# Kernel optimization log

Hardware: AMD Instinct MI355X
Metric: run time of the kernel (lower is better)

Reference implementation:

```python
import jax, jax.numpy as jnp
import numpy as np

B, T, C, H = 4, 2048, 1024, 16
HD = C // H


def setup_inputs() -> dict:
    key = jax.random.key(0)
    k1, k2, k3, k4 = jax.random.split(key, 4)
    x = jax.random.normal(k1, (B, T, C), dtype=jnp.float32)
    pad_mask = jnp.ones((B, T), dtype=jnp.int32)
    # Linear weights stored as (in, out); torch Linear uses W.T so math is identical.
    w_attn = jax.random.normal(k2, (C, 3 * C), dtype=jnp.float32) * (1.0 / np.sqrt(C))
    w_proj = jax.random.normal(k3, (C, C), dtype=jnp.float32) * (1.0 / np.sqrt(C))
    b_proj = jax.random.normal(k4, (C,), dtype=jnp.float32) * 0.01
    return {"x": x, "pad_mask": pad_mask, "w_attn": w_attn, "w_proj": w_proj, "b_proj": b_proj}


def reference(x, pad_mask, w_attn, w_proj, b_proj):
    Bx, Tx, Cx = x.shape
    hd = Cx // H
    qkv = x @ w_attn                                  # (B,T,3C)
    q, k, v = jnp.split(qkv, 3, axis=2)
    # (B,T,C) -> (B,H,T,hd)
    q = q.reshape(Bx, Tx, H, hd).transpose(0, 2, 1, 3)
    k = k.reshape(Bx, Tx, H, hd).transpose(0, 2, 1, 3)
    v = v.reshape(Bx, Tx, H, hd).transpose(0, 2, 1, 3)
    att = jnp.einsum('bhqd,bhkd->bhqk', q, k) * (1.0 / np.sqrt(hd))
    causal = jnp.tril(jnp.ones((Tx, Tx), dtype=bool))[None, None]       # (1,1,T,T)
    keep = causal & (pad_mask[:, None, None, :] != 0)                   # (B,1,T,T) broadcast
    att = jnp.where(keep, att, -jnp.inf)
    att = jax.nn.softmax(att, axis=-1)
    # dropout p=0.0 (eval) -> identity
    y = jnp.einsum('bhqk,bhkd->bhqd', att, v)
    y = y.transpose(0, 2, 1, 3).reshape(Bx, Tx, Cx)
    return y @ w_proj + b_proj
```

## Files before the change

kernel.cpp:

```cpp
#include <hip/hip_runtime.h>
#include <hip/hip_bf16.h>


using short8  = __attribute__((ext_vector_type(8))) short;
using short4_ = __attribute__((ext_vector_type(4))) short;
using uint2_  = __attribute__((ext_vector_type(2))) unsigned int;
using float4_ = __attribute__((ext_vector_type(4))) float;

#define Bb   4
#define Tt   2048
#define Cc   1024
#define Hh   16
#define HDd  64

__device__ __forceinline__ float bf2f(unsigned short u) {
    union { float f; unsigned int i; } x; x.i = ((unsigned int)u) << 16; return x.f;
}
__device__ __forceinline__ unsigned short f2bf(float f) {
    union { float f; unsigned int i; } x; x.f = f;
    unsigned int r = x.i + 0x7fff + ((x.i >> 16) & 1);
    return (unsigned short)(r >> 16);
}
__device__ __forceinline__ unsigned int cvtpk_bf16(float lo, float hi) {
    unsigned int r;
    asm("v_cvt_pk_bf16_f32 %0, %1, %2" : "=v"(r) : "v"(lo), "v"(hi));
    return r;
}
__device__ __forceinline__ float4_ bmfma(short8 a, short8 b, float4_ c) {
    return __builtin_amdgcn_mfma_f32_16x16x32_bf16(a, b, c, 0, 0, 0);
}
__device__ __forceinline__ float ex2(float x) {
    return __builtin_amdgcn_exp2f(x);
}
__device__ __forceinline__ void gl2lds16(const unsigned short* g, unsigned short* l) {
    __builtin_amdgcn_global_load_lds(
        (const __attribute__((address_space(1))) void*)g,
        (__attribute__((address_space(3))) void*)l, 16, 0, 0);
}

__global__ __launch_bounds__(256) void convert_f32_bf16(
    const float* __restrict__ in, unsigned short* __restrict__ out)
{
    size_t idx = ((size_t)blockIdx.x * 256 + threadIdx.x) * 8;
    float4_ f0 = *(const float4_*)&in[idx];
    float4_ f1 = *(const float4_*)&in[idx + 4];
    short8 h;
    h[0] = (short)f2bf(f0[0]); h[1] = (short)f2bf(f0[1]);
    h[2] = (short)f2bf(f0[2]); h[3] = (short)f2bf(f0[3]);
    h[4] = (short)f2bf(f1[0]); h[5] = (short)f2bf(f1[1]);
    h[6] = (short)f2bf(f1[2]); h[7] = (short)f2bf(f1[3]);
    *(short8*)&out[idx] = h;
}

__global__ __launch_bounds__(256) void transpose_f32_bf16(
    const float* __restrict__ in, unsigned short* __restrict__ out,
    int R, int Ccols)
{
    __shared__ unsigned short tile[32][33];
    int c0 = blockIdx.x * 32, r0 = blockIdx.y * 32;
    int tx = threadIdx.x & 31, ty = threadIdx.x >> 5;
    for (int o = 0; o < 32; o += 8)
        tile[ty + o][tx] = f2bf(in[(size_t)(r0 + ty + o) * Ccols + c0 + tx]);
    __syncthreads();
    for (int o = 0; o < 32; o += 8)
        out[(size_t)(c0 + ty + o) * R + r0 + tx] = tile[tx][ty + o];
}

#define GBK 64

__device__ __forceinline__ void gemm128_main(
    const unsigned short* __restrict__ A, const unsigned short* __restrict__ Bt,
    int K, int m0, int n0,
    unsigned short* As, unsigned short* Bs, float4_ acc[4][4], bool swapT)
{
    int tid  = threadIdx.x;
    int wave = tid >> 6, lane = tid & 63;
    int wm = (wave >> 1) * 64, wn = (wave & 1) * 64;
    int lr = lane & 15, lg = lane >> 4;
    int srow = tid >> 3;
    int scol = (tid & 7) * 8;

    for (int k0 = 0; k0 < K; k0 += GBK) {
        #pragma unroll
        for (int j = 0; j < 4; j++) {
            int row = j * 32 + srow;
            gl2lds16(&A [(size_t)(m0 + row) * K + k0 + scol], &As[row * GBK + scol]);
            gl2lds16(&Bt[(size_t)(n0 + row) * K + k0 + scol], &Bs[row * GBK + scol]);
        }
        __syncthreads();
        #pragma unroll
        for (int ks = 0; ks < GBK; ks += 32) {
            short8 af[4], bf[4];
            #pragma unroll
            for (int i = 0; i < 4; i++) {
                af[i] = *(const short8*)&As[(wm + i * 16 + lr) * GBK + ks + lg * 8];
                bf[i] = *(const short8*)&Bs[(wn + i * 16 + lr) * GBK + ks + lg * 8];
            }
            if (!swapT) {
                #pragma unroll
                for (int i = 0; i < 4; i++)
                    #pragma unroll
                    for (int j = 0; j < 4; j++)
                        acc[i][j] = bmfma(af[i], bf[j], acc[i][j]);
            } else {
                #pragma unroll
                for (int i = 0; i < 4; i++)
                    #pragma unroll
                    for (int j = 0; j < 4; j++)
                        acc[i][j] = bmfma(bf[i], af[j], acc[i][j]);
            }
        }
        __syncthreads();
    }
}

__device__ __forceinline__ void supertile_remap(int& m0, int& n0)
{
    int bx = blockIdx.x, by = blockIdx.y;
    int mt = ((by & 7) << 3) | (bx & 7);
    int nt = ((by >> 3) << 3) | (bx >> 3);
    m0 = mt * 128; n0 = nt * 128;
}

__global__ __launch_bounds__(256) void gemm_qkv(
    const unsigned short* __restrict__ A,
    const unsigned short* __restrict__ Bt,
    unsigned short* __restrict__ Q,
    unsigned short* __restrict__ Ko,
    unsigned short* __restrict__ V)
{
    __shared__ unsigned short As[128 * GBK];
    __shared__ unsigned short Bs[128 * GBK];
    int m0, n0;
    supertile_remap(m0, n0);
    bool vblk = (n0 >= 2048);
    float4_ acc[4][4] = {};
    gemm128_main(A, Bt, 1024, m0, n0, As, Bs, acc, vblk);

    int lane = threadIdx.x & 63, wave = threadIdx.x >> 6;
    int wm = (wave >> 1) * 64, wn = (wave & 1) * 64;
    int lr = lane & 15, lg = lane >> 4;
    if (!vblk) {
        #pragma unroll
        for (int i = 0; i < 4; i++)
            #pragma unroll
            for (int j = 0; j < 4; j++) {
                int n = n0 + wn + 16 * j + lr;
                int which = n >> 10;
                int c = n & 1023;
                int h = c >> 6, d = c & 63;
                unsigned short* dst = (which == 0) ? Q : Ko;
                float sc2 = (which == 0) ? 0.1803368801f : 1.0f;
                #pragma unroll
                for (int r = 0; r < 4; r++) {
                    int m = m0 + wm + 16 * i + lg * 4 + r;
                    int b = m >> 11, t = m & 2047;
                    dst[(((size_t)(b * Hh + h) * Tt) + t) * HDd + d] = f2bf(acc[i][j][r] * sc2);
                }
            }
    } else {
        #pragma unroll
        for (int i = 0; i < 4; i++)
            #pragma unroll
            for (int j = 0; j < 4; j++) {
                int m = m0 + wm + 16 * j + lr;
                int b = m >> 11, t = m & 2047;
                #pragma unroll
                for (int r = 0; r < 4; r++) {
                    int n = n0 + wn + 16 * i + lg * 4 + r;
                    int c = n - 2048;
                    int h = c >> 6, d = c & 63;
                    V[(((size_t)(b * Hh + h) * HDd) + d) * Tt + t] = f2bf(acc[i][j][r]);
                }
            }
    }
}

__global__ __launch_bounds__(256) void gemm_proj(
    const unsigned short* __restrict__ A,
    const unsigned short* __restrict__ Bt,
    const float* __restrict__ bias,
    float* __restrict__ Out)
{
    __shared__ unsigned short As[128 * GBK];
    __shared__ unsigned short Bs[128 * GBK];
    int m0, n0;
    supertile_remap(m0, n0);
    float4_ acc[4][4] = {};
    gemm128_main(A, Bt, 1024, m0, n0, As, Bs, acc, false);

    int lane = threadIdx.x & 63, wave = threadIdx.x >> 6;
    int wm = (wave >> 1) * 64, wn = (wave & 1) * 64;
    int lr = lane & 15, lg = lane >> 4;
    #pragma unroll
    for (int i = 0; i < 4; i++)
        #pragma unroll
        for (int j = 0; j < 4; j++) {
            int n = n0 + wn + 16 * j + lr;
            float bv = bias[n];
            #pragma unroll
            for (int r = 0; r < 4; r++) {
                int m = m0 + wm + 16 * i + lg * 4 + r;
                Out[(size_t)m * 1024 + n] = acc[i][j][r] + bv;
            }
        }
}

#define DPAD 72

__global__ __launch_bounds__(256) void attn_fwd(
    const unsigned short* __restrict__ Q,
    const unsigned short* __restrict__ Kg,
    const unsigned short* __restrict__ Vg,
    const int* __restrict__ pad,
    unsigned short* __restrict__ Y)
{
    __shared__ unsigned short smem[4 * 64 * DPAD];

    int flat = blockIdx.x;
    int qb = 31 - (flat >> 6);
    int bh = flat & 63;
    int b  = bh >> 4, h = bh & 15;
    const size_t base = (size_t)bh * Tt * HDd;
    int tid  = threadIdx.x;
    int wave = tid >> 6, lane = tid & 63;
    int lr = lane & 15, lg = lane >> 4;
    int q0 = qb * 64 + wave * 16;
    const int* padRow = pad + b * Tt;

    int r8 = tid >> 3;
    int c8 = (tid & 7) * 8;

    short8 qf0 = *(const short8*)&Q[base + (size_t)(q0 + lr) * HDd + lg * 8];
    short8 qf1 = *(const short8*)&Q[base + (size_t)(q0 + lr) * HDd + 32 + lg * 8];

    float m_i = -1e30f, l_i = 0.f;
    float4_ o_acc[4];
    #pragma unroll
    for (int dt = 0; dt < 4; dt++) o_acc[dt] = (float4_){0.f, 0.f, 0.f, 0.f};

    int ebase = (lg & 1) * 4;
    int hnib  = lg >> 1;
    int q2    = (2 * lr) & 7;

    short8 kr0 = *(const short8*)&Kg[base + (size_t)r8 * HDd + c8];
    short8 kr1 = *(const short8*)&Kg[base + (size_t)(r8 + 32) * HDd + c8];
    short8 vr0 = *(const short8*)&Vg[base + (size_t)r8 * Tt + c8];
    short8 vr1 = *(const short8*)&Vg[base + (size_t)(r8 + 32) * Tt + c8];
    int pvld = padRow[lane];

    for (int kt = 0; kt <= qb; kt++) {
        int cur = kt & 1;
        unsigned short* Kt = smem + cur * (2 * 64 * DPAD);
        unsigned short* Vt = Kt + 64 * DPAD;
        *(short8*)&Kt[r8 * DPAD + c8]        = kr0;
        *(short8*)&Kt[(r8 + 32) * DPAD + c8] = kr1;
        *(short8*)&Vt[r8 * DPAD + c8]        = vr0;
        *(short8*)&Vt[(r8 + 32) * DPAD + c8] = vr1;
        unsigned long long pm = __ballot(pvld != 0);
        __syncthreads();

        if (kt < qb) {
            int k1 = kt * 64 + 64;
            kr0 = *(const short8*)&Kg[base + (size_t)(k1 + r8) * HDd + c8];
            kr1 = *(const short8*)&Kg[base + (size_t)(k1 + r8 + 32) * HDd + c8];
            vr0 = *(const short8*)&Vg[base + (size_t)r8 * Tt + k1 + c8];
            vr1 = *(const short8*)&Vg[base + (size_t)(r8 + 32) * Tt + k1 + c8];
            pvld = padRow[k1 + lane];
        }

        float4_ s[4];
        #pragma unroll
        for (int nt = 0; nt < 4; nt++) {
            short8 kf0 = *(const short8*)&Kt[(nt * 16 + lr) * DPAD + lg * 8];
            short8 kf1 = *(const short8*)&Kt[(nt * 16 + lr) * DPAD + 32 + lg * 8];
            float4_ a = (float4_){0.f, 0.f, 0.f, 0.f};
            a = bmfma(kf0, qf0, a);
            a = bmfma(kf1, qf1, a);
            s[nt] = a;
        }
        if (kt == qb) {
            #pragma unroll
            for (int nt = 0; nt < 4; nt++)
                #pragma unroll
                for (int r = 0; r < 4; r++) {
                    int kl = nt * 16 + lg * 4 + r;
                    bool kpv = (pm >> kl) & 1ull;
                    if (!kpv || kl > wave * 16 + lr) s[nt][r] = -1e30f;
                }
        } else if (pm != ~0ull) {
            #pragma unroll
            for (int nt = 0; nt < 4; nt++)
                #pragma unroll
                for (int r = 0; r < 4; r++) {
                    int kl = nt * 16 + lg * 4 + r;
                    bool kpv = (pm >> kl) & 1ull;
                    s[nt][r] = kpv ? s[nt][r] : -1e30f;
                }
        }
        float v = fmaxf(fmaxf(s[0][0], s[0][1]), fmaxf(s[0][2], s[0][3]));
        #pragma unroll
        for (int nt = 1; nt < 4; nt++)
            v = fmaxf(v, fmaxf(fmaxf(s[nt][0], s[nt][1]), fmaxf(s[nt][2], s[nt][3])));
        v = fmaxf(v, __shfl_xor(v, 16, 64));
        v = fmaxf(v, __shfl_xor(v, 32, 64));
        bool need = __any(v > m_i + 8.0f);
        float alpha = 1.0f;
        if (need) {
            float m_new = fmaxf(m_i, v);
            alpha = ex2(m_i - m_new);
            m_i = m_new;
        }
        float rsum = 0.f;
        #pragma unroll
        for (int nt = 0; nt < 4; nt++)
            #pragma unroll
            for (int r = 0; r < 4; r++) {
                float p = ex2(s[nt][r] - m_i);
                s[nt][r] = p;
                rsum += p;
            }
        rsum += __shfl_xor(rsum, 16, 64);
        rsum += __shfl_xor(rsum, 32, 64);
        l_i = l_i * alpha + rsum;

        if (need) {
            #pragma unroll
            for (int r = 0; r < 4; r++) {
                float ar = __shfl(alpha, (lg << 2) + r, 64);
                #pragma unroll
                for (int dt = 0; dt < 4; dt++)
                    o_acc[dt][r] *= ar;
            }
        }

        __syncthreads();

        unsigned short* Pw = &Kt[wave * 16 * DPAD];
        #pragma unroll
        for (int nt = 0; nt < 4; nt++) {
            uint2_ w;
            w[0] = cvtpk_bf16(s[nt][0], s[nt][1]);
            w[1] = cvtpk_bf16(s[nt][2], s[nt][3]);
            int p = (2 * nt + hnib - q2) & 7;
            *(uint2_*)&Pw[lr * DPAD + p * 8 + ebase] = w;
        }
        short8 pf0 = *(const short8*)&Pw[lr * DPAD + (((lg - q2) & 7) << 3)];
        short8 pf1 = *(const short8*)&Pw[lr * DPAD + (((4 + lg - q2) & 7) << 3)];
        #pragma unroll
        for (int dt = 0; dt < 4; dt++) {
            int d = dt * 16 + lr;
            short8 vf0 = *(const short8*)&Vt[d * DPAD + lg * 8];
            short8 vf1 = *(const short8*)&Vt[d * DPAD + 32 + lg * 8];
            o_acc[dt] = bmfma(pf0, vf0, o_acc[dt]);
            o_acc[dt] = bmfma(pf1, vf1, o_acc[dt]);
        }
    }

    #pragma unroll
    for (int r = 0; r < 4; r++) {
        float lr_ = __shfl(l_i, (lg << 2) + r, 64);
        int qrow = q0 + lg * 4 + r;
        #pragma unroll
        for (int dt = 0; dt < 4; dt++)
            Y[((size_t)b * Tt + qrow) * Cc + h * HDd + dt * 16 + lr] =
                f2bf(o_acc[dt][r] / lr_);
    }
}

extern "C" void kernel_launch(void* const* d_in, const int* in_sizes, int n_in,
                              void* d_out, int out_size, void* d_ws, size_t ws_size,
                              hipStream_t stream)
{
    const float* x      = (const float*)d_in[0];
    const int*   pad    = (const int*)d_in[1];
    const float* w_attn = (const float*)d_in[2];
    const float* w_proj = (const float*)d_in[3];
    const float* b_proj = (const float*)d_in[4];
    float*       out    = (float*)d_out;

    unsigned short* Wta = (unsigned short*)d_ws;
    unsigned short* Wtp = Wta + (size_t)3072 * 1024;
    unsigned short* Xb  = Wtp + (size_t)1024 * 1024;
    unsigned short* Yb  = Xb;
    unsigned short* Qb  = Xb + (size_t)8192 * 1024;
    unsigned short* Kb  = Qb + (size_t)Bb * Hh * Tt * HDd;
    unsigned short* Vb  = Kb + (size_t)Bb * Hh * Tt * HDd;

    convert_f32_bf16<<<dim3(4096), 256, 0, stream>>>(x, Xb);
    transpose_f32_bf16<<<dim3(3072 / 32, 1024 / 32), 256, 0, stream>>>(w_attn, Wta, 1024, 3072);
    transpose_f32_bf16<<<dim3(1024 / 32, 1024 / 32), 256, 0, stream>>>(w_proj, Wtp, 1024, 1024);
    gemm_qkv<<<dim3(8192 / 128, 3072 / 128), 256, 0, stream>>>(Xb, Wta, Qb, Kb, Vb);
    attn_fwd<<<dim3(2048), 256, 0, stream>>>(Qb, Kb, Vb, pad, Yb);
    gemm_proj<<<dim3(8192 / 128, 1024 / 128), 256, 0, stream>>>(Yb, Wtp, b_proj, out);
}
```

Measured before the change: 275.9 us.

## Process two 16-row query tiles per wave in attention to reuse K/V tiles

The attention kernel now gives each block 128 query rows instead of 64, so each wave handles two 16-row query tiles (A and B) against every K/V tile staged in shared memory. This halves the number of blocks and the global-to-LDS K/V traffic per query row, and makes more MFMA work available per sync. Causal masking now covers the last two diagonal tiles using a key offset. The cost is roughly double the accumulator and score registers per thread, which may lower occupancy. Parallelism also drops to 1024 blocks, with coarser causal load imbalance.

After: 282.8 us. 2.5% more time.

```diff
diff --git a/kernel.cpp b/kernel.cpp
--- a/kernel.cpp
+++ b/kernel.cpp
@@ -218,30 +218,37 @@
     __shared__ unsigned short smem[4 * 64 * DPAD];
 
     int flat = blockIdx.x;
-    int qb = 31 - (flat >> 6);
+    int qb = 15 - (flat >> 6);
     int bh = flat & 63;
     int b  = bh >> 4, h = bh & 15;
     const size_t base = (size_t)bh * Tt * HDd;
     int tid  = threadIdx.x;
     int wave = tid >> 6, lane = tid & 63;
     int lr = lane & 15, lg = lane >> 4;
-    int q0 = qb * 64 + wave * 16;
+    int qwA = qb * 128 + wave * 32;
     const int* padRow = pad + b * Tt;
 
     int r8 = tid >> 3;
     int c8 = (tid & 7) * 8;
 
-    short8 qf0 = *(const short8*)&Q[base + (size_t)(q0 + lr) * HDd + lg * 8];
-    short8 qf1 = *(const short8*)&Q[base + (size_t)(q0 + lr) * HDd + 32 + lg * 8];
-
-    float m_i = -1e30f, l_i = 0.f;
-    float4_ o_acc[4];
+    short8 qfA0 = *(const short8*)&Q[base + (size_t)(qwA + lr) * HDd + lg * 8];
+    short8 qfA1 = *(const short8*)&Q[base + (size_t)(qwA + lr) * HDd + 32 + lg * 8];
+    short8 qfB0 = *(const short8*)&Q[base + (size_t)(qwA + 16 + lr) * HDd + lg * 8];
+    short8 qfB1 = *(const short8*)&Q[base + (size_t)(qwA + 16 + lr) * HDd + 32 + lg * 8];
+
+    float mA = -1e30f, lA = 0.f, mB = -1e30f, lB = 0.f;
+    float4_ oA[4], oB[4];
     #pragma unroll
-    for (int dt = 0; dt < 4; dt++) o_acc[dt] = (float4_){0.f, 0.f, 0.f, 0.f};
+    for (int dt = 0; dt < 4; dt++) {
+        oA[dt] = (float4_){0.f, 0.f, 0.f, 0.f};
+        oB[dt] = (float4_){0.f, 0.f, 0.f, 0.f};
+    }
 
     int ebase = (lg & 1) * 4;
     int hnib  = lg >> 1;
     int q2    = (2 * lr) & 7;
+
+    int NT = 2 * qb + 2;
 
     short8 kr0 = *(const short8*)&Kg[base + (size_t)r8 * HDd + c8];
     short8 kr1 = *(const short8*)&Kg[base + (size_t)(r8 + 32) * HDd + c8];
@@ -249,7 +256,7 @@
     short8 vr1 = *(const short8*)&Vg[base + (size_t)(r8 + 32) * Tt + c8];
     int pvld = padRow[lane];
 
-    for (int kt = 0; kt <= qb; kt++) {
+    for (int kt = 0; kt < NT; kt++) {
         int cur = kt & 1;
         unsigned short* Kt = smem + cur * (2 * 64 * DPAD);
         unsigned short* Vt = Kt + 64 * DPAD;
@@ -260,7 +267,7 @@
         unsigned long long pm = __ballot(pvld != 0);
         __syncthreads();
 
-        if (kt < qb) {
+        if (kt < NT - 1) {
             int k1 = kt * 64 + 64;
             kr0 = *(const short8*)&Kg[base + (size_t)(k1 + r8) * HDd + c8];
             kr1 = *(const short8*)&Kg[base + (size_t)(k1 + r8 + 32) * HDd + c8];
@@ -269,24 +276,30 @@
             pvld = padRow[k1 + lane];
         }
 
-        float4_ s[4];
+        float4_ sA[4], sB[4];
         #pragma unroll
         for (int nt = 0; nt < 4; nt++) {
             short8 kf0 = *(const short8*)&Kt[(nt * 16 + lr) * DPAD + lg * 8];
             short8 kf1 = *(const short8*)&Kt[(nt * 16 + lr) * DPAD + 32 + lg * 8];
             float4_ a = (float4_){0.f, 0.f, 0.f, 0.f};
-            a = bmfma(kf0, qf0, a);
-            a = bmfma(kf1, qf1, a);
-            s[nt] = a;
-        }
-        if (kt == qb) {
+            a = bmfma(kf0, qfA0, a);
+            a = bmfma(kf1, qfA1, a);
+            sA[nt] = a;
+            float4_ c = (float4_){0.f, 0.f, 0.f, 0.f};
+            c = bmfma(kf0, qfB0, c);
+            c = bmfma(kf1, qfB1, c);
+            sB[nt] = c;
+        }
+        if (kt >= 2 * qb) {
+            int dk = (kt - 2 * qb) * 64;
             #pragma unroll
             for (int nt = 0; nt < 4; nt++)
                 #pragma unroll
                 for (int r = 0; r < 4; r++) {
                     int kl = nt * 16 + lg * 4 + r;
                     bool kpv = (pm >> kl) & 1ull;
-                    if (!kpv || kl > wave * 16 + lr) s[nt][r] = -1e30f;
+                    if (!kpv || dk + kl > wave * 32 + lr)      sA[nt][r] = -1e30f;
+                    if (!kpv || dk + kl > wave * 32 + 16 + lr) sB[nt][r] = -1e30f;
                 }
         } else if (pm != ~0ull) {
             #pragma unroll
@@ -295,43 +308,59 @@
                 for (int r = 0; r < 4; r++) {
                     int kl = nt * 16 + lg * 4 + r;
                     bool kpv = (pm >> kl) & 1ull;
-                    s[nt][r] = kpv ? s[nt][r] : -1e30f;
+                    if (!kpv) { sA[nt][r] = -1e30f; sB[nt][r] = -1e30f; }
                 }
         }
-        float v = fmaxf(fmaxf(s[0][0], s[0][1]), fmaxf(s[0][2], s[0][3]));
-        #pragma unroll
-        for (int nt = 1; nt < 4; nt++)
-            v = fmaxf(v, fmaxf(fmaxf(s[nt][0], s[nt][1]), fmaxf(s[nt][2], s[nt][3])));
-        v = fmaxf(v, __shfl_xor(v, 16, 64));
-        v = fmaxf(v, __shfl_xor(v, 32, 64));
-        bool need = __any(v > m_i + 8.0f);
-        float alpha = 1.0f;
+        float vA = fmaxf(fmaxf(sA[0][0], sA[0][1]), fmaxf(sA[0][2], sA[0][3]));
+        float vB = fmaxf(fmaxf(sB[0][0], sB[0][1]), fmaxf(sB[0][2], sB[0][3]));
+        #pragma unroll
+        for (int nt = 1; nt < 4; nt++) {
+            vA = fmaxf(vA, fmaxf(fmaxf(sA[nt][0], sA[nt][1]), fmaxf(sA[nt][2], sA[nt][3])));
+            vB = fmaxf(vB, fmaxf(fmaxf(sB[nt][0], sB[nt][1]), fmaxf(sB[nt][2], sB[nt][3])));
+        }
+        vA = fmaxf(vA, __shfl_xor(vA, 16, 64));
+        vA = fmaxf(vA, __shfl_xor(vA, 32, 64));
+        vB = fmaxf(vB, __shfl_xor(vB, 16, 64));
+        vB = fmaxf(vB, __shfl_xor(vB, 32, 64));
+        bool need = __any(vA > mA + 8.0f) || __any(vB > mB + 8.0f);
+        float aA = 1.0f, aB = 1.0f;
         if (need) {
-            float m_new = fmaxf(m_i, v);
-            alpha = ex2(m_i - m_new);
-            m_i = m_new;
-        }
-        float rsum = 0.f;
+            float mnA = fmaxf(mA, vA); aA = ex2(mA - mnA); mA = mnA;
+            float mnB = fmaxf(mB, vB); aB = ex2(mB - mnB); mB = mnB;
+        }
+        float rsA = 0.f, rsB = 0.f;
         #pragma unroll
         for (int nt = 0; nt < 4; nt++)
             #pragma unroll
             for (int r = 0; r < 4; r++) {
-                float p = ex2(s[nt][r] - m_i);
-                s[nt][r] = p;
-                rsum += p;
-            }
-        rsum += __shfl_xor(rsum, 16, 64);
-        rsum += __shfl_xor(rsum, 32, 64);
-        l_i = l_i * alpha + rsum;
-
+                float pA = ex2(sA[nt][r] - mA); sA[nt][r] = pA; rsA += pA;
+                float pB = ex2(sB[nt][r] - mB); sB[nt][r] = pB; rsB += pB;
+            }
+        rsA += __shfl_xor(rsA, 16, 64);
+        rsA += __shfl_xor(rsA, 32, 64);
+        rsB += __shfl_xor(rsB, 16, 64);
+        rsB += __shfl_xor(rsB, 32, 64);
+        lA = lA * aA + rsA;
+        lB = lB * aB + rsB;
         if (need) {
             #pragma unroll
             for (int r = 0; r < 4; r++) {
-                float ar = __shfl(alpha, (lg << 2) + r, 64);
-                #pragma unroll
-                for (int dt = 0; dt < 4; dt++)
-                    o_acc[dt][r] *= ar;
-            }
+                float arA = __shfl(aA, (lg << 2) + r, 64);
+                float arB = __shfl(aB, (lg << 2) + r, 64);
+                #pragma unroll
+                for (int dt = 0; dt < 4; dt++) {
+                    oA[dt][r] *= arA;
+                    oB[dt][r] *= arB;
+                }
+            }
+        }
+        uint2_ wPA[4], wPB[4];
+        #pragma unroll
+        for (int nt = 0; nt < 4; nt++) {
+            wPA[nt][0] = cvtpk_bf16(sA[nt][0], sA[nt][1]);
+            wPA[nt][1] = cvtpk_bf16(sA[nt][2], sA[nt][3]);
+            wPB[nt][0] = cvtpk_bf16(sB[nt][0], sB[nt][1]);
+            wPB[nt][1] = cvtpk_bf16(sB[nt][2], sB[nt][3]);
         }
 
         __syncthreads();
@@ -339,32 +368,43 @@
         unsigned short* Pw = &Kt[wave * 16 * DPAD];
         #pragma unroll
         for (int nt = 0; nt < 4; nt++) {
-            uint2_ w;
-            w[0] = cvtpk_bf16(s[nt][0], s[nt][1]);
-            w[1] = cvtpk_bf16(s[nt][2], s[nt][3]);
             int p = (2 * nt + hnib - q2) & 7;
-            *(uint2_*)&Pw[lr * DPAD + p * 8 + ebase] = w;
-        }
-        short8 pf0 = *(const short8*)&Pw[lr * DPAD + (((lg - q2) & 7) << 3)];
-        short8 pf1 = *(const short8*)&Pw[lr * DPAD + (((4 + lg - q2) & 7) << 3)];
+            *(uint2_*)&Pw[lr * DPAD + p * 8 + ebase] = wPA[nt];
+        }
+        short8 pfA0 = *(const short8*)&Pw[lr * DPAD + (((lg - q2) & 7) << 3)];
+        short8 pfA1 = *(const short8*)&Pw[lr * DPAD + (((4 + lg - q2) & 7) << 3)];
+        #pragma unroll
+        for (int nt = 0; nt < 4; nt++) {
+            int p = (2 * nt + hnib - q2) & 7;
+            *(uint2_*)&Pw[lr * DPAD + p * 8 + ebase] = wPB[nt];
+        }
+        short8 pfB0 = *(const short8*)&Pw[lr * DPAD + (((lg - q2) & 7) << 3)];
+        short8 pfB1 = *(const short8*)&Pw[lr * DPAD + (((4 + lg - q2) & 7) << 3)];
         #pragma unroll
         for (int dt = 0; dt < 4; dt++) {
             int d = dt * 16 + lr;
             short8 vf0 = *(const short8*)&Vt[d * DPAD + lg * 8];
             short8 vf1 = *(const short8*)&Vt[d * DPAD + 32 + lg * 8];
-            o_acc[dt] = bmfma(pf0, vf0, o_acc[dt]);
-            o_acc[dt] = bmfma(pf1, vf1, o_acc[dt]);
+            oA[dt] = bmfma(pfA0, vf0, oA[dt]);
+            oA[dt] = bmfma(pfA1, vf1, oA[dt]);
+            oB[dt] = bmfma(pfB0, vf0, oB[dt]);
+            oB[dt] = bmfma(pfB1, vf1, oB[dt]);
         }
     }
 
     #pragma unroll
     for (int r = 0; r < 4; r++) {
-        float lr_ = __shfl(l_i, (lg << 2) + r, 64);
-        int qrow = q0 + lg * 4 + r;
-        #pragma unroll
-        for (int dt = 0; dt < 4; dt++)
-            Y[((size_t)b * Tt + qrow) * Cc + h * HDd + dt * 16 + lr] =
-                f2bf(o_acc[dt][r] / lr_);
+        float lAr = __shfl(lA, (lg << 2) + r, 64);
+        float lBr = __shfl(lB, (lg << 2) + r, 64);
+        int qrA = qwA + lg * 4 + r;
+        int qrB = qwA + 16 + lg * 4 + r;
+        #pragma unroll
+        for (int dt = 0; dt < 4; dt++) {
+            Y[((size_t)b * Tt + qrA) * Cc + h * HDd + dt * 16 + lr] =
+                f2bf(oA[dt][r] / lAr);
+            Y[((size_t)b * Tt + qrB) * Cc + h * HDd + dt * 16 + lr] =
+                f2bf(oB[dt][r] / lBr);
+        }
     }
 }
 
@@ -391,6 +431,6 @@
     transpose_f32_bf16<<<dim3(3072 / 32, 1024 / 32), 256, 0, stream>>>(w_attn, Wta, 1024, 3072);
     transpose_f32_bf16<<<dim3(1024 / 32, 1024 / 32), 256, 0, stream>>>(w_proj, Wtp, 1024, 1024);
     gemm_qkv<<<dim3(8192 / 128, 3072 / 128), 256, 0, stream>>>(Xb, Wta, Qb, Kb, Vb);
-    attn_fwd<<<dim3(2048), 256, 0, stream>>>(Qb, Kb, Vb, pad, Yb);
+    attn_fwd<<<dim3(1024), 256, 0, stream>>>(Qb, Kb, Vb, pad, Yb);
     gemm_proj<<<dim3(8192 / 128, 1024 / 128), 256, 0, stream>>>(Yb, Wtp, b_proj, out);
 }
```

## Load K/V MFMA fragments directly from global memory, drop LDS staging

Applied to the files above, without the earlier changes.

The attention kernel stops staging K and V tiles in shared memory with register prefetch and block-wide barriers. Each wave now reads its K and V MFMA fragments straight from global memory, and shared memory holds only the per-wave P tile. This removes the two __syncthreads per iteration and the LDS write/read traffic, and the smaller LDS footprint may allow more blocks per CU. In exchange, each of the four waves loads the same K/V data separately, which quadruples global/L2 traffic, and the software prefetch overlap is lost.

Result: slower. 452.5 us (+64.0%).

```diff
diff --git a/kernel.cpp b/kernel.cpp
--- a/kernel.cpp
+++ b/kernel.cpp
@@ -215,7 +215,7 @@
     const int* __restrict__ pad,
     unsigned short* __restrict__ Y)
 {
-    __shared__ unsigned short smem[4 * 64 * DPAD];
+    __shared__ unsigned short Psm[4 * 16 * DPAD];
 
     int flat = blockIdx.x;
     int qb = 31 - (flat >> 6);
@@ -227,9 +227,7 @@
     int lr = lane & 15, lg = lane >> 4;
     int q0 = qb * 64 + wave * 16;
     const int* padRow = pad + b * Tt;
-
-    int r8 = tid >> 3;
-    int c8 = (tid & 7) * 8;
+    unsigned short* Pw = &Psm[wave * 16 * DPAD];
 
     short8 qf0 = *(const short8*)&Q[base + (size_t)(q0 + lr) * HDd + lg * 8];
     short8 qf1 = *(const short8*)&Q[base + (size_t)(q0 + lr) * HDd + 32 + lg * 8];
@@ -243,42 +241,23 @@
     int hnib  = lg >> 1;
     int q2    = (2 * lr) & 7;
 
-    short8 kr0 = *(const short8*)&Kg[base + (size_t)r8 * HDd + c8];
-    short8 kr1 = *(const short8*)&Kg[base + (size_t)(r8 + 32) * HDd + c8];
-    short8 vr0 = *(const short8*)&Vg[base + (size_t)r8 * Tt + c8];
-    short8 vr1 = *(const short8*)&Vg[base + (size_t)(r8 + 32) * Tt + c8];
-    int pvld = padRow[lane];
-
     for (int kt = 0; kt <= qb; kt++) {
-        int cur = kt & 1;
-        unsigned short* Kt = smem + cur * (2 * 64 * DPAD);
-        unsigned short* Vt = Kt + 64 * DPAD;
-        *(short8*)&Kt[r8 * DPAD + c8]        = kr0;
-        *(short8*)&Kt[(r8 + 32) * DPAD + c8] = kr1;
-        *(short8*)&Vt[r8 * DPAD + c8]        = vr0;
-        *(short8*)&Vt[(r8 + 32) * DPAD + c8] = vr1;
-        unsigned long long pm = __ballot(pvld != 0);
-        __syncthreads();
-
-        if (kt < qb) {
-            int k1 = kt * 64 + 64;
-            kr0 = *(const short8*)&Kg[base + (size_t)(k1 + r8) * HDd + c8];
-            kr1 = *(const short8*)&Kg[base + (size_t)(k1 + r8 + 32) * HDd + c8];
-            vr0 = *(const short8*)&Vg[base + (size_t)r8 * Tt + k1 + c8];
-            vr1 = *(const short8*)&Vg[base + (size_t)(r8 + 32) * Tt + k1 + c8];
-            pvld = padRow[k1 + lane];
-        }
+        int k0 = kt * 64;
 
         float4_ s[4];
         #pragma unroll
         for (int nt = 0; nt < 4; nt++) {
-            short8 kf0 = *(const short8*)&Kt[(nt * 16 + lr) * DPAD + lg * 8];
-            short8 kf1 = *(const short8*)&Kt[(nt * 16 + lr) * DPAD + 32 + lg * 8];
+            const unsigned short* kp = &Kg[base + (size_t)(k0 + nt * 16 + lr) * HDd];
+            short8 kf0 = *(const short8*)&kp[lg * 8];
+            short8 kf1 = *(const short8*)&kp[32 + lg * 8];
             float4_ a = (float4_){0.f, 0.f, 0.f, 0.f};
             a = bmfma(kf0, qf0, a);
             a = bmfma(kf1, qf1, a);
             s[nt] = a;
         }
+        int pvld = padRow[k0 + lane];
+        unsigned long long pm = __ballot(pvld != 0);
+
         if (kt == qb) {
             #pragma unroll
             for (int nt = 0; nt < 4; nt++)
@@ -334,9 +313,6 @@
             }
         }
 
-        __syncthreads();
-
-        unsigned short* Pw = &Kt[wave * 16 * DPAD];
         #pragma unroll
         for (int nt = 0; nt < 4; nt++) {
             uint2_ w;
@@ -349,9 +325,9 @@
         short8 pf1 = *(const short8*)&Pw[lr * DPAD + (((4 + lg - q2) & 7) << 3)];
         #pragma unroll
         for (int dt = 0; dt < 4; dt++) {
-            int d = dt * 16 + lr;
-            short8 vf0 = *(const short8*)&Vt[d * DPAD + lg * 8];
-            short8 vf1 = *(const short8*)&Vt[d * DPAD + 32 + lg * 8];
+            const unsigned short* vp = &Vg[base + (size_t)(dt * 16 + lr) * Tt + k0];
+            short8 vf0 = *(const short8*)&vp[lg * 8];
+            short8 vf1 = *(const short8*)&vp[32 + lg * 8];
             o_acc[dt] = bmfma(pf0, vf0, o_acc[dt]);
             o_acc[dt] = bmfma(pf1, vf1, o_acc[dt]);
         }
```
